# Performance work log

Hardware: AMD Instinct MI355X
Metric: run time of the kernel (lower is better)

Reference implementation:

```python
import jax, jax.numpy as jnp
import numpy as np

B, NQ, NK, DQ, DK, DV, H = 8, 256, 512, 256, 256, 256, 64
NEG = -1e6


def setup_inputs() -> dict:
    key = jax.random.key(0)
    k1, k2, k3, k4, k5, k6, k7 = jax.random.split(key, 7)
    return {
        "queries": jax.random.normal(k1, (B, NQ, DQ), dtype=jnp.float32),
        "keys": jax.random.normal(k2, (B, NK, DK), dtype=jnp.float32),
        "values": jax.random.normal(k3, (B, NK, DV), dtype=jnp.float32),
        "valid_lens": jax.random.randint(k4, (B,), 1, NK + 1),
        "Wq": jax.random.normal(k5, (DQ, H), dtype=jnp.float32) / np.sqrt(DQ),
        "Wk": jax.random.normal(k6, (DK, H), dtype=jnp.float32) / np.sqrt(DK),
        "wv": jax.random.normal(k7, (H,), dtype=jnp.float32) / np.sqrt(H),
    }


def reference(queries, keys, values, valid_lens, Wq, Wk, wv):
    # project: [B,NQ,H], [B,NK,H]
    q = jnp.einsum("bqd,dh->bqh", queries, Wq)
    k = jnp.einsum("bkd,dh->bkh", keys, Wk)
    # additive features: [B,NQ,NK,H] -> tanh -> reduce with w_v -> scores [B,NQ,NK]
    features = jnp.tanh(q[:, :, None, :] + k[:, None, :, :])
    scores = jnp.einsum("bqkh,h->bqk", features, wv)
    # masked softmax over key axis (per-batch valid_lens)
    mask = jnp.arange(NK)[None, None, :] < valid_lens[:, None, None]
    scores = jnp.where(mask, scores, NEG)
    attn = jax.nn.softmax(scores, axis=-1)
    # dropout p=0 (eval) -> identity; weighted sum of values [B,NQ,DV]
    return jnp.einsum("bqk,bkv->bqv", attn, values)
```

## Files before the change

### kernel.cpp

```cpp
#include <hip/hip_runtime.h>
#include <hip/hip_bf16.h>

constexpr int B  = 8;
constexpr int NQ = 256;
constexpr int NK = 512;
constexpr int D  = 256;
constexpr int DV = 256;
constexpr int H  = 64;
constexpr float NEG = -1e6f;
constexpr float LOG2E = 1.4426950408889634f;
constexpr float CSCALE = 2.f * LOG2E;

constexpr int RPB = 16;

__global__ __launch_bounds__(256) void proj_kernel(
    const float* __restrict__ queries, const float* __restrict__ keys,
    const float* __restrict__ Wq, const float* __restrict__ Wk,
    float* __restrict__ qp, float* __restrict__ kp)
{
    const int r0 = blockIdx.x * RPB;
    const bool isQ = (r0 < B * NQ);
    const float* src = isQ ? queries + (size_t)r0 * D
                           : keys + (size_t)(r0 - B * NQ) * D;
    const float* W   = isQ ? Wq : Wk;
    float* out       = isQ ? qp + (size_t)r0 * H
                           : kp + (size_t)(r0 - B * NQ) * H;

    __shared__ __align__(16) float rows[RPB][D];
#pragma unroll
    for (int j = 0; j < 4; ++j)
        ((float4*)&rows[0][0])[threadIdx.x + j * 256] =
            ((const float4*)src)[threadIdx.x + j * 256];
    __syncthreads();

    const int h = threadIdx.x & 63;
    const int g = threadIdx.x >> 6;
    float s0 = 0.f, s1 = 0.f, s2 = 0.f, s3 = 0.f;
#pragma unroll 2
    for (int d4 = 0; d4 < D / 4; ++d4) {
        float w0 = W[(d4 * 4 + 0) * H + h];
        float w1 = W[(d4 * 4 + 1) * H + h];
        float w2 = W[(d4 * 4 + 2) * H + h];
        float w3 = W[(d4 * 4 + 3) * H + h];
        float4 ra = *(const float4*)&rows[g][d4 * 4];
        float4 rb = *(const float4*)&rows[g + 4][d4 * 4];
        float4 rc = *(const float4*)&rows[g + 8][d4 * 4];
        float4 rd = *(const float4*)&rows[g + 12][d4 * 4];
        s0 = fmaf(ra.x, w0, s0);  s1 = fmaf(rb.x, w0, s1);
        s2 = fmaf(rc.x, w0, s2);  s3 = fmaf(rd.x, w0, s3);
        s0 = fmaf(ra.y, w1, s0);  s1 = fmaf(rb.y, w1, s1);
        s2 = fmaf(rc.y, w1, s2);  s3 = fmaf(rd.y, w1, s3);
        s0 = fmaf(ra.z, w2, s0);  s1 = fmaf(rb.z, w2, s1);
        s2 = fmaf(rc.z, w2, s2);  s3 = fmaf(rd.z, w2, s3);
        s0 = fmaf(ra.w, w3, s0);  s1 = fmaf(rb.w, w3, s1);
        s2 = fmaf(rc.w, w3, s2);  s3 = fmaf(rd.w, w3, s3);
    }
    out[g * H + h]        = s0 * CSCALE;
    out[(g + 4) * H + h]  = s1 * CSCALE;
    out[(g + 8) * H + h]  = s2 * CSCALE;
    out[(g + 12) * H + h] = s3 * CSCALE;
}

constexpr int KT   = 128;
constexpr int KPAD = 68;
constexpr int QPAD = 68;

#define FMA4(acc, a, v) \
    acc.x = fmaf(a, v.x, acc.x); acc.y = fmaf(a, v.y, acc.y); \
    acc.z = fmaf(a, v.z, acc.z); acc.w = fmaf(a, v.w, acc.w);

__global__ __launch_bounds__(512, 4) void attn_kernel(
    const float* __restrict__ qp, const float* __restrict__ kp,
    const float* __restrict__ values, const int* __restrict__ valid_lens,
    const float* __restrict__ wv, float* __restrict__ out)
{
    const int b    = blockIdx.x & 7;
    const int q0   = (blockIdx.x >> 3) * 4;
    const int t    = threadIdx.x;
    const int w    = t >> 6;
    const int l    = t & 63;
    const int qloc = w >> 1;
    const int half = w & 1;
    const int qsc  = l >> 4;
    const int kidx = l & 15;

    __shared__ __align__(16) float kT[KT * KPAD];
    __shared__ __align__(16) float qv[4][QPAD];
    __shared__ __align__(16) float w2[H];
    __shared__ __align__(16) float sc[4][NK];

    if (half == 0)
        qv[qloc][l] = qp[((size_t)b * NQ + q0 + qloc) * H + l];

    const float wvl = wv[l];
    float swv = wvl;
#pragma unroll
    for (int off = 32; off > 0; off >>= 1) swv += __shfl_xor(swv, off);
    if (w == 0) w2[l] = -2.f * wvl;

    const int vlen = valid_lens[b];

    for (int kt = 0; kt < NK / KT; ++kt) {
        const int kg = kt * KT + w * 16 + kidx;
        if (kt * KT < vlen) {
            __syncthreads();
            const float* src = kp + ((size_t)b * NK + kt * KT) * H;
#pragma unroll
            for (int j = 0; j < 4; ++j) {
                int idx4 = t + j * 512;
                int kk = idx4 >> 4;
                int hb = (idx4 & 15) * 4;
                float4 v = ((const float4*)src)[idx4];
                *(float4*)&kT[kk * KPAD + hb] = v;
            }
            __syncthreads();

            const float* qrow = &qv[qsc][0];
            const float* krow = &kT[(w * 16 + kidx) * KPAD];
            float s0 = 0.f;
#pragma unroll
            for (int h4 = 0; h4 < H / 4; ++h4) {
                float4 kk = *(const float4*)&krow[h4 * 4];
                float4 qq = *(const float4*)&qrow[h4 * 4];
                float4 ww = *(const float4*)&w2[h4 * 4];
                float r;
                r = __builtin_amdgcn_rcpf(__builtin_amdgcn_exp2f(qq.x + kk.x) + 1.f);
                s0 = fmaf(ww.x, r, s0);
                r = __builtin_amdgcn_rcpf(__builtin_amdgcn_exp2f(qq.y + kk.y) + 1.f);
                s0 = fmaf(ww.y, r, s0);
                r = __builtin_amdgcn_rcpf(__builtin_amdgcn_exp2f(qq.z + kk.z) + 1.f);
                s0 = fmaf(ww.z, r, s0);
                r = __builtin_amdgcn_rcpf(__builtin_amdgcn_exp2f(qq.w + kk.w) + 1.f);
                s0 = fmaf(ww.w, r, s0);
            }
            sc[qsc][kg] = (kg < vlen) ? (s0 + swv) : NEG;
        } else {
            sc[qsc][kg] = NEG;
        }
    }
    __syncthreads();

    float vals[8];
    float m = -INFINITY;
#pragma unroll
    for (int j = 0; j < 8; ++j) {
        vals[j] = sc[qloc][l + j * 64];
        m = fmaxf(m, vals[j]);
    }
#pragma unroll
    for (int off = 32; off > 0; off >>= 1) m = fmaxf(m, __shfl_xor(m, off));
    float sum = 0.f;
#pragma unroll
    for (int j = 0; j < 8; ++j) {
        float p = __builtin_amdgcn_exp2f((vals[j] - m) * LOG2E);
        vals[j] = p;
        sum += p;
    }
#pragma unroll
    for (int off = 32; off > 0; off >>= 1) sum += __shfl_xor(sum, off);
    const float rinv = __builtin_amdgcn_rcpf(sum);
    if (half == 0) {
        sc[qloc][l + 0 * 64] = vals[0] * rinv;
        sc[qloc][l + 1 * 64] = vals[1] * rinv;
        sc[qloc][l + 2 * 64] = vals[2] * rinv;
        sc[qloc][l + 3 * 64] = vals[3] * rinv;
    } else {
        sc[qloc][l + 4 * 64] = vals[4] * rinv;
        sc[qloc][l + 5 * 64] = vals[5] * rinv;
        sc[qloc][l + 6 * 64] = vals[6] * rinv;
        sc[qloc][l + 7 * 64] = vals[7] * rinv;
    }
    __syncthreads();

    float4 acc0 = {0,0,0,0}, acc1 = {0,0,0,0}, acc2 = {0,0,0,0}, acc3 = {0,0,0,0};
    const float* Vb = values + (size_t)b * NK * DV;
    const int nchunks = (vlen + 3) >> 2;
    for (int c = w; c < nchunks; c += 8) {
        const int k = 4 * c;
        float4 a0 = *(const float4*)&sc[0][k];
        float4 a1 = *(const float4*)&sc[1][k];
        float4 a2 = *(const float4*)&sc[2][k];
        float4 a3 = *(const float4*)&sc[3][k];
        const float* vr = Vb + (size_t)k * DV + 4 * l;
        float4 v0 = *(const float4*)(vr);
        float4 v1 = *(const float4*)(vr + DV);
        float4 v2 = *(const float4*)(vr + 2 * DV);
        float4 v3 = *(const float4*)(vr + 3 * DV);
        FMA4(acc0, a0.x, v0); FMA4(acc0, a0.y, v1); FMA4(acc0, a0.z, v2); FMA4(acc0, a0.w, v3);
        FMA4(acc1, a1.x, v0); FMA4(acc1, a1.y, v1); FMA4(acc1, a1.z, v2); FMA4(acc1, a1.w, v3);
        FMA4(acc2, a2.x, v0); FMA4(acc2, a2.y, v1); FMA4(acc2, a2.z, v2); FMA4(acc2, a2.w, v3);
        FMA4(acc3, a3.x, v0); FMA4(acc3, a3.y, v1); FMA4(acc3, a3.z, v2); FMA4(acc3, a3.w, v3);
    }

    float* pt = kT;
    *(float4*)&pt[(w * 4 + 0) * 256 + 4 * l] = acc0;
    *(float4*)&pt[(w * 4 + 1) * 256 + 4 * l] = acc1;
    *(float4*)&pt[(w * 4 + 2) * 256 + 4 * l] = acc2;
    *(float4*)&pt[(w * 4 + 3) * 256 + 4 * l] = acc3;
    __syncthreads();

    if (w < 4) {
        float4 r = {0,0,0,0};
#pragma unroll
        for (int s = 0; s < 8; ++s) {
            float4 p = *(const float4*)&pt[(s * 4 + w) * 256 + 4 * l];
            r.x += p.x; r.y += p.y; r.z += p.z; r.w += p.w;
        }
        *(float4*)&out[((size_t)b * NQ + q0 + w) * DV + 4 * l] = r;
    }
}

extern "C" void kernel_launch(void* const* d_in, const int* in_sizes, int n_in,
                              void* d_out, int out_size, void* d_ws, size_t ws_size,
                              hipStream_t stream) {
    const float* queries    = (const float*)d_in[0];
    const float* keys       = (const float*)d_in[1];
    const float* values     = (const float*)d_in[2];
    const int*   valid_lens = (const int*)d_in[3];
    const float* Wq         = (const float*)d_in[4];
    const float* Wk         = (const float*)d_in[5];
    const float* wv         = (const float*)d_in[6];
    float* out = (float*)d_out;

    float* qp = (float*)d_ws;
    float* kp = qp + (size_t)B * NQ * H;

    proj_kernel<<<(B * NQ + B * NK) / RPB, 256, 0, stream>>>(
        queries, keys, Wq, Wk, qp, kp);

    attn_kernel<<<B * (NQ / 4), 512, 0, stream>>>(
        qp, kp, values, valid_lens, wv, out);
}
```

Measured before the change: 103.5 us.

## Double-buffer key tiles in LDS with register prefetch in attention kernel

The score loop now keeps two LDS key-tile buffers. It loads the next tile into registers while computing the current one, writes it to the other buffer, and uses one barrier per tile instead of two. Tiles past valid_len are set to NEG up front and the loop runs only over valid tiles. Block indexing changes to batch-major, and launch bounds drop to 2 blocks per CU. The doubled LDS footprint and extra prefetch registers lower occupancy, which may offset the overlap gain in this exp/rcp-bound loop.

```diff
diff --git a/kernel.cpp b/kernel.cpp
--- a/kernel.cpp
+++ b/kernel.cpp
@@ -69,13 +69,13 @@
     acc.x = fmaf(a, v.x, acc.x); acc.y = fmaf(a, v.y, acc.y); \
     acc.z = fmaf(a, v.z, acc.z); acc.w = fmaf(a, v.w, acc.w);
 
-__global__ __launch_bounds__(512, 4) void attn_kernel(
+__global__ __launch_bounds__(512, 2) void attn_kernel(
     const float* __restrict__ qp, const float* __restrict__ kp,
     const float* __restrict__ values, const int* __restrict__ valid_lens,
     const float* __restrict__ wv, float* __restrict__ out)
 {
-    const int b    = blockIdx.x & 7;
-    const int q0   = (blockIdx.x >> 3) * 4;
+    const int b    = blockIdx.x >> 6;
+    const int q0   = (blockIdx.x & 63) * 4;
     const int t    = threadIdx.x;
     const int w    = t >> 6;
     const int l    = t & 63;
@@ -84,7 +84,7 @@
     const int qsc  = l >> 4;
     const int kidx = l & 15;
 
-    __shared__ __align__(16) float kT[KT * KPAD];
+    __shared__ __align__(16) float kT[2][KT * KPAD];
     __shared__ __align__(16) float qv[4][QPAD];
     __shared__ __align__(16) float w2[H];
     __shared__ __align__(16) float sc[4][NK];
@@ -98,47 +98,65 @@
     for (int off = 32; off > 0; off >>= 1) swv += __shfl_xor(swv, off);
     if (w == 0) w2[l] = -2.f * wvl;
 
-    const int vlen = valid_lens[b];
-
-    for (int kt = 0; kt < NK / KT; ++kt) {
+    const int vlen   = valid_lens[b];
+    const int ntiles = (vlen + KT - 1) / KT;
+
+    for (int kt = ntiles; kt < NK / KT; ++kt)
+        sc[qsc][kt * KT + w * 16 + kidx] = NEG;
+
+    const float* kpb = kp + (size_t)b * NK * H;
+
+    float4 pre[4];
+#pragma unroll
+    for (int j = 0; j < 4; ++j)
+        pre[j] = ((const float4*)kpb)[t + j * 512];
+#pragma unroll
+    for (int j = 0; j < 4; ++j) {
+        int idx4 = t + j * 512;
+        *(float4*)&kT[0][(idx4 >> 4) * KPAD + (idx4 & 15) * 4] = pre[j];
+    }
+    __syncthreads();
+
+    for (int kt = 0; kt < ntiles; ++kt) {
+        const int cur = kt & 1;
+        const bool more = (kt + 1 < ntiles);
+        if (more) {
+            const float* src = kpb + (size_t)(kt + 1) * KT * H;
+#pragma unroll
+            for (int j = 0; j < 4; ++j)
+                pre[j] = ((const float4*)src)[t + j * 512];
+        }
+
         const int kg = kt * KT + w * 16 + kidx;
-        if (kt * KT < vlen) {
-            __syncthreads();
-            const float* src = kp + ((size_t)b * NK + kt * KT) * H;
+        const float* qrow = &qv[qsc][0];
+        const float* krow = &kT[cur][(w * 16 + kidx) * KPAD];
+        float s0 = 0.f;
+#pragma unroll
+        for (int h4 = 0; h4 < H / 4; ++h4) {
+            float4 kk = *(const float4*)&krow[h4 * 4];
+            float4 qq = *(const float4*)&qrow[h4 * 4];
+            float4 ww = *(const float4*)&w2[h4 * 4];
+            float r;
+            r = __builtin_amdgcn_rcpf(__builtin_amdgcn_exp2f(qq.x + kk.x) + 1.f);
+            s0 = fmaf(ww.x, r, s0);
+            r = __builtin_amdgcn_rcpf(__builtin_amdgcn_exp2f(qq.y + kk.y) + 1.f);
+            s0 = fmaf(ww.y, r, s0);
+            r = __builtin_amdgcn_rcpf(__builtin_amdgcn_exp2f(qq.z + kk.z) + 1.f);
+            s0 = fmaf(ww.z, r, s0);
+            r = __builtin_amdgcn_rcpf(__builtin_amdgcn_exp2f(qq.w + kk.w) + 1.f);
+            s0 = fmaf(ww.w, r, s0);
+        }
+        sc[qsc][kg] = (kg < vlen) ? (s0 + swv) : NEG;
+
+        if (more) {
 #pragma unroll
             for (int j = 0; j < 4; ++j) {
                 int idx4 = t + j * 512;
-                int kk = idx4 >> 4;
-                int hb = (idx4 & 15) * 4;
-                float4 v = ((const float4*)src)[idx4];
-                *(float4*)&kT[kk * KPAD + hb] = v;
+                *(float4*)&kT[cur ^ 1][(idx4 >> 4) * KPAD + (idx4 & 15) * 4] = pre[j];
             }
-            __syncthreads();
-
-            const float* qrow = &qv[qsc][0];
-            const float* krow = &kT[(w * 16 + kidx) * KPAD];
-            float s0 = 0.f;
-#pragma unroll
-            for (int h4 = 0; h4 < H / 4; ++h4) {
-                float4 kk = *(const float4*)&krow[h4 * 4];
-                float4 qq = *(const float4*)&qrow[h4 * 4];
-                float4 ww = *(const float4*)&w2[h4 * 4];
-                float r;
-                r = __builtin_amdgcn_rcpf(__builtin_amdgcn_exp2f(qq.x + kk.x) + 1.f);
-                s0 = fmaf(ww.x, r, s0);
-                r = __builtin_amdgcn_rcpf(__builtin_amdgcn_exp2f(qq.y + kk.y) + 1.f);
-                s0 = fmaf(ww.y, r, s0);
-                r = __builtin_amdgcn_rcpf(__builtin_amdgcn_exp2f(qq.z + kk.z) + 1.f);
-                s0 = fmaf(ww.z, r, s0);
-                r = __builtin_amdgcn_rcpf(__builtin_amdgcn_exp2f(qq.w + kk.w) + 1.f);
-                s0 = fmaf(ww.w, r, s0);
-            }
-            sc[qsc][kg] = (kg < vlen) ? (s0 + swv) : NEG;
-        } else {
-            sc[qsc][kg] = NEG;
-        }
-    }
-    __syncthreads();
+        }
+        __syncthreads();
+    }
 
     float vals[8];
     float m = -INFINITY;
@@ -192,7 +210,7 @@
         FMA4(acc3, a3.x, v0); FMA4(acc3, a3.y, v1); FMA4(acc3, a3.z, v2); FMA4(acc3, a3.w, v3);
     }
 
-    float* pt = kT;
+    float* pt = &kT[0][0];
     *(float4*)&pt[(w * 4 + 0) * 256 + 4 * l] = acc0;
     *(float4*)&pt[(w * 4 + 1) * 256 + 4 * l] = acc1;
     *(float4*)&pt[(w * 4 + 2) * 256 + 4 * l] = acc2;
```

Measured after the change: 110.0 us. 6.3% more time.
